# Kernel optimization log

Hardware: AMD Instinct MI355X
Metric: run time of the kernel (lower is better)

The kernel has to match this reference:

```python
import jax, jax.numpy as jnp
import numpy as np

N_NODES = 50000


def gcn_conv(h, W, b, src, dst, n_nodes):
    # PyG GCNConv: h' = D^{-1/2} (A + I) D^{-1/2} (h @ W) + b
    h = h @ W  # [N, out]
    deg = jax.ops.segment_sum(jnp.ones_like(dst, dtype=h.dtype), dst, num_segments=n_nodes)
    dinv = jnp.where(deg > 0, jax.lax.rsqrt(deg), 0.0)  # [N]
    norm = dinv[src] * dinv[dst]  # [E]
    msg = h[src] * norm[:, None]  # [E, out]
    out = jax.ops.segment_sum(msg, dst, num_segments=n_nodes)
    return out + b


def setup_inputs() -> dict:
    key = jax.random.key(0)
    ks = jax.random.split(key, 12)
    N, E, P, D, H = N_NODES, 1600000, 200000, 128, 128
    s = lambda fan_in: 1.0 / np.sqrt(fan_in)
    return {
        "x": jax.random.normal(ks[0], (N, D), dtype=jnp.float32),
        "edge_index": jax.random.randint(ks[1], (2, E), 0, N, dtype=jnp.int32),
        "drug_pairs": jax.random.randint(ks[2], (P, 2), 0, N, dtype=jnp.int32),
        "W1": jax.random.normal(ks[3], (D, H), dtype=jnp.float32) * s(D),
        "b1": jnp.zeros((H,), dtype=jnp.float32),
        "W2": jax.random.normal(ks[4], (H, H), dtype=jnp.float32) * s(H),
        "b2": jnp.zeros((H,), dtype=jnp.float32),
        "Wh1": jax.random.normal(ks[5], (2 * H, H), dtype=jnp.float32) * s(2 * H),
        "bh1": jnp.zeros((H,), dtype=jnp.float32),
        "Wh2": jax.random.normal(ks[6], (H, 1), dtype=jnp.float32) * s(H),
        "bh2": jnp.zeros((1,), dtype=jnp.float32),
    }


def reference(x, edge_index, drug_pairs, W1, b1, W2, b2, Wh1, bh1, Wh2, bh2):
    n = x.shape[0]
    # add self-loops once (GCNConv default add_self_loops=True)
    loop = jnp.arange(n, dtype=edge_index.dtype)
    src = jnp.concatenate([edge_index[0], loop])
    dst = jnp.concatenate([edge_index[1], loop])

    h = jax.nn.relu(gcn_conv(x, W1, b1, src, dst, n))  # dropout = identity (eval)
    h = jax.nn.relu(gcn_conv(h, W2, b2, src, dst, n))

    combined = jnp.concatenate([h[drug_pairs[:, 0]], h[drug_pairs[:, 1]]], axis=1)  # [P, 2H]
    out = jax.nn.relu(combined @ Wh1 + bh1) @ Wh2 + bh2  # [P, 1]
    return out
```

## Files before the change

kernel.cpp:

```cpp
#include <hip/hip_runtime.h>
#include <hip/hip_fp16.h>


#define BSH 9
#define BSZ (1 << BSH)
#define MSB 4096
#define XPAD 132
#define HB 256

typedef __attribute__((ext_vector_type(8))) short bf16x8;
typedef __attribute__((ext_vector_type(8))) _Float16 f16x8;
typedef __attribute__((ext_vector_type(4))) float f32x4;
typedef __attribute__((ext_vector_type(4))) int i32x4;

__device__ __forceinline__ void acc8(uint4 u, float4& lo, float4& hi) {
  float2 f0 = __half22float2(((const __half2*)&u)[0]);
  float2 f1 = __half22float2(((const __half2*)&u)[1]);
  float2 f2 = __half22float2(((const __half2*)&u)[2]);
  float2 f3 = __half22float2(((const __half2*)&u)[3]);
  lo.x += f0.x; lo.y += f0.y; lo.z += f1.x; lo.w += f1.y;
  hi.x += f2.x; hi.y += f2.y; hi.z += f3.x; hi.w += f3.y;
}

__device__ __forceinline__ void split8(const float* v, bf16x8& hi, bf16x8& lo) {
#pragma unroll
  for (int j = 0; j < 8; ++j) {
    unsigned u = __float_as_uint(v[j]);
    hi[j] = (short)(u >> 16);
    float lf = v[j] - __uint_as_float(u & 0xffff0000u);
    lo[j] = (short)(__float_as_uint(lf) >> 16);
  }
}

__global__ __launch_bounds__(256) void k_prep_hist(
    const float* __restrict__ W1, const float* __restrict__ W2,
    const float* __restrict__ Wh1, short* __restrict__ fragH,
    short* __restrict__ fragL,
    const int* __restrict__ dst, int* __restrict__ gcnt, int e, int kb) {
  if (blockIdx.x >= 32) {
    __shared__ int h4[512];
    int bid = blockIdx.x - 32;
    int tid = threadIdx.x, wid = tid >> 6;
    for (int t = tid; t < 512; t += 256) h4[t] = 0;
    __syncthreads();
    const i32x4* dst4 = (const i32x4*)dst;
    int ne4 = e >> 2;
    const int STR = HB * 256;
    int i = bid * 256 + tid;
    for (; i < ne4 - STR; i += 2 * STR) {
      i32x4 a = __builtin_nontemporal_load(&dst4[i]);
      i32x4 b = __builtin_nontemporal_load(&dst4[i + STR]);
      atomicAdd(&h4[wid * 128 + (a.x >> BSH)], 1);
      atomicAdd(&h4[wid * 128 + (a.y >> BSH)], 1);
      atomicAdd(&h4[wid * 128 + (a.z >> BSH)], 1);
      atomicAdd(&h4[wid * 128 + (a.w >> BSH)], 1);
      atomicAdd(&h4[wid * 128 + (b.x >> BSH)], 1);
      atomicAdd(&h4[wid * 128 + (b.y >> BSH)], 1);
      atomicAdd(&h4[wid * 128 + (b.z >> BSH)], 1);
      atomicAdd(&h4[wid * 128 + (b.w >> BSH)], 1);
    }
    for (; i < ne4; i += STR) {
      i32x4 a = __builtin_nontemporal_load(&dst4[i]);
      atomicAdd(&h4[wid * 128 + (a.x >> BSH)], 1);
      atomicAdd(&h4[wid * 128 + (a.y >> BSH)], 1);
      atomicAdd(&h4[wid * 128 + (a.z >> BSH)], 1);
      atomicAdd(&h4[wid * 128 + (a.w >> BSH)], 1);
    }
    if (bid == 0 && tid < (e & 3)) {
      int d = dst[(ne4 << 2) + tid];
      atomicAdd(&h4[wid * 128 + (d >> BSH)], 1);
    }
    __syncthreads();
    if (tid < kb)
      atomicAdd(&gcnt[tid], h4[tid] + h4[128 + tid] + h4[256 + tid] + h4[384 + tid]);
    return;
  }
  int g = blockIdx.x * 256 + threadIdx.x;
  int w = g >> 11;
  int rem = g & 2047;
  int lane = rem & 63;
  int ts = rem >> 6;
  int t = ts >> 2, s = ts & 3;
  int n = (t << 4) + (lane & 15);
  int k0 = s * 32 + (lane >> 4) * 8;
  const float* W = (w == 0) ? W1 : (w == 1) ? W2 : (w == 2) ? Wh1 : (Wh1 + 128 * 128);
  short h[8], l[8];
#pragma unroll
  for (int j = 0; j < 8; ++j) {
    float x = W[(k0 + j) * 128 + n];
    if (w == 0) {
      unsigned u = __float_as_uint(x);
      h[j] = (short)(u >> 16);
      float lf = x - __uint_as_float(u & 0xffff0000u);
      l[j] = (short)(__float_as_uint(lf) >> 16);
    } else {
      __half hh = __float2half(x);
      h[j] = __half_as_short(hh);
      l[j] = __half_as_short(__float2half(x - __half2float(hh)));
    }
  }
  ((int4*)fragH)[g] = *(int4*)h;
  ((int4*)fragL)[g] = *(int4*)l;
}

__device__ __forceinline__ void gemm1_body(
    const float* __restrict__ X, const short* __restrict__ fragH,
    const short* __restrict__ fragL, __half* __restrict__ C16, int n,
    int bid, float* sX) {
  int tid = threadIdx.x;
  int row0 = bid * 64;
  const float2* X2 = (const float2*)(X + (size_t)row0 * 128);
#pragma unroll
  for (int it = 0; it < 16; ++it) {
    int t = it * 256 + tid;
    int r = t >> 6, c2 = t & 63;
    int gr = row0 + r;
    float2 v = (gr < n) ? X2[t] : make_float2(0.f, 0.f);
    *(float2*)&sX[r * XPAD + c2 * 2] = v;
  }
  __syncthreads();
  int wid = tid >> 6, lane = tid & 63;
  int r0 = row0 + wid * 16;
  if (r0 >= n) return;
  int m = lane & 15, quad = lane >> 4;
  const float* xrow = sX + (wid * 16 + m) * XPAD;
  f32x4 acc[8];
#pragma unroll
  for (int t = 0; t < 8; ++t) acc[t] = (f32x4)(0.f);
  const int4* FH = (const int4*)fragH;
  const int4* FL = (const int4*)fragL;
#pragma unroll
  for (int s = 0; s < 4; ++s) {
    int k0 = s * 32 + quad * 8;
    float xv[8];
    *(float2*)&xv[0] = *(const float2*)(xrow + k0);
    *(float2*)&xv[2] = *(const float2*)(xrow + k0 + 2);
    *(float2*)&xv[4] = *(const float2*)(xrow + k0 + 4);
    *(float2*)&xv[6] = *(const float2*)(xrow + k0 + 6);
    bf16x8 ah, al;
    split8(xv, ah, al);
#pragma unroll
    for (int t = 0; t < 8; ++t) {
      int idx = (t * 4 + s) * 64 + lane;
      bf16x8 bh = *(const bf16x8*)&FH[idx];
      bf16x8 bl = *(const bf16x8*)&FL[idx];
      acc[t] = __builtin_amdgcn_mfma_f32_16x16x32_bf16(ah, bh, acc[t], 0, 0, 0);
      acc[t] = __builtin_amdgcn_mfma_f32_16x16x32_bf16(al, bh, acc[t], 0, 0, 0);
      acc[t] = __builtin_amdgcn_mfma_f32_16x16x32_bf16(ah, bl, acc[t], 0, 0, 0);
    }
  }
#pragma unroll
  for (int t = 0; t < 8; ++t) {
#pragma unroll
    for (int r = 0; r < 4; ++r) {
      int row = r0 + quad * 4 + r;
      C16[(size_t)row * 128 + t * 16 + m] = __float2half(acc[t][r]);
    }
  }
}

__device__ __forceinline__ void multisplit_body(
    const int* __restrict__ src, const int* __restrict__ dst,
    const int* __restrict__ gcnt, int* __restrict__ gcur,
    int* __restrict__ tmp, int e, int kb, int bid, int* lds) {
  int* h4 = lds;
  int* off = lds + 512;
  int* sbase = lds + 1024;
  int* ws = lds + 1152;
  int tid = threadIdx.x, wid = tid >> 6, lane = tid & 63;
  for (int t = tid; t < 512; t += 256) h4[t] = 0;
  __syncthreads();
  int i0 = bid * MSB + tid;
  int d[16], rk[16];
#pragma unroll
  for (int u = 0; u < 16; ++u) {
    int i = i0 + u * 256;
    if (i < e) {
      d[u] = __builtin_nontemporal_load(&dst[i]);
      rk[u] = atomicAdd(&h4[wid * 128 + (d[u] >> BSH)], 1);
    }
  }
  __syncthreads();
  int tot = 0;
  if (tid < 128) {
    int c0 = h4[tid], c1 = h4[128 + tid], c2 = h4[256 + tid], c3 = h4[384 + tid];
    off[tid] = 0; off[128 + tid] = c0;
    off[256 + tid] = c0 + c1; off[384 + tid] = c0 + c1 + c2;
    tot = c0 + c1 + c2 + c3;
  }
  int v = (tid < 128 && tid < kb) ? gcnt[tid] : 0;
  int orig = v;
#pragma unroll
  for (int o = 1; o < 64; o <<= 1) {
    int u = __shfl_up(v, o, 64);
    if (lane >= o) v += u;
  }
  if (lane == 63 && wid < 2) ws[wid] = v;
  __syncthreads();
  if (tid < 128) sbase[tid] = ((wid == 1) ? ws[0] : 0) + v - orig;
  __syncthreads();
  if (tid < kb && tot > 0) sbase[tid] += atomicAdd(&gcur[tid], tot);
  __syncthreads();
#pragma unroll
  for (int u = 0; u < 16; ++u) {
    int i = i0 + u * 256;
    if (i < e) {
      int s = __builtin_nontemporal_load(&src[i]);
      int k = d[u] >> BSH;
      tmp[sbase[k] + off[wid * 128 + k] + rk[u]] = ((d[u] & (BSZ - 1)) << 16) | s;
    }
  }
}

__global__ __launch_bounds__(256) void k_ms_gemm1(
    const int* __restrict__ src, const int* __restrict__ dst,
    const int* __restrict__ gcnt, int* __restrict__ gcur,
    int* __restrict__ tmp, int e, int kb, int msblocks,
    const float* __restrict__ X, const short* __restrict__ fragH,
    const short* __restrict__ fragL, __half* __restrict__ C16, int n) {
  __shared__ float sX[64 * XPAD];
  if ((int)blockIdx.x < msblocks) {
    multisplit_body(src, dst, gcnt, gcur, tmp, e, kb, blockIdx.x, (int*)sX);
    return;
  }
  gemm1_body(X, fragH, fragL, C16, n, blockIdx.x - msblocks, sX);
}

__global__ __launch_bounds__(512) void k_bucket_build(
    const int* __restrict__ tmp, const int* __restrict__ gcnt,
    int* __restrict__ rowptr, float* __restrict__ dinv,
    unsigned short* __restrict__ colarr, __half* __restrict__ g16,
    int n, int kb, int e) {
  __shared__ int dl[BSZ], cl[BSZ], sbase[128], ws[8];
  __shared__ float sdi[BSZ];
  int t = threadIdx.x, b = blockIdx.x;
  int lane = t & 63, w = t >> 6;
  int v = (t < 128 && t < kb) ? gcnt[t] : 0;
  int orig0 = v;
#pragma unroll
  for (int o = 1; o < 64; o <<= 1) {
    int u = __shfl_up(v, o, 64);
    if (lane >= o) v += u;
  }
  if (lane == 63 && w < 2) ws[w] = v;
  dl[t] = 0;
  __syncthreads();
  if (t < 128) sbase[t] = ((w == 1) ? ws[0] : 0) + v - orig0;
  __syncthreads();
  int s0 = sbase[b];
  int s1 = s0 + gcnt[b];
  {
    int j = s0 + t;
    for (; j < s1 - 3584; j += 4096) {
      int v0 = tmp[j];
      int v1 = tmp[j + 512];
      int v2 = tmp[j + 1024];
      int v3 = tmp[j + 1536];
      int v4 = tmp[j + 2048];
      int v5 = tmp[j + 2560];
      int v6 = tmp[j + 3072];
      int v7 = tmp[j + 3584];
      atomicAdd(&dl[((unsigned)v0) >> 16], 1);
      atomicAdd(&dl[((unsigned)v1) >> 16], 1);
      atomicAdd(&dl[((unsigned)v2) >> 16], 1);
      atomicAdd(&dl[((unsigned)v3) >> 16], 1);
      atomicAdd(&dl[((unsigned)v4) >> 16], 1);
      atomicAdd(&dl[((unsigned)v5) >> 16], 1);
      atomicAdd(&dl[((unsigned)v6) >> 16], 1);
      atomicAdd(&dl[((unsigned)v7) >> 16], 1);
    }
    for (; j < s1; j += 512)
      atomicAdd(&dl[((unsigned)tmp[j]) >> 16], 1);
  }
  __syncthreads();
  int dv = dl[t], orig = dv;
#pragma unroll
  for (int o = 1; o < 64; o <<= 1) {
    int u = __shfl_up(dv, o, 64);
    if (lane >= o) dv += u;
  }
  if (lane == 63) ws[w] = dv;
  __syncthreads();
  if (t == 0) {
    int a = 0;
#pragma unroll
    for (int k = 0; k < 8; ++k) { int x = ws[k]; ws[k] = a; a += x; }
  }
  __syncthreads();
  int ex = ws[w] + dv - orig;
  cl[t] = ex;
  int node = (b << BSH) + t;
  float di = rsqrtf((float)(orig + 1));
  sdi[t] = di;
  if (node < n) {
    rowptr[node] = s0 + ex;
    dinv[node] = di;
  }
  if (b == kb - 1 && t == 0) rowptr[n] = e;
  __syncthreads();
  {
    int j = s0 + t;
    for (; j < s1 - 3584; j += 4096) {
      int p0 = tmp[j];
      int p1 = tmp[j + 512];
      int p2 = tmp[j + 1024];
      int p3 = tmp[j + 1536];
      int p4 = tmp[j + 2048];
      int p5 = tmp[j + 2560];
      int p6 = tmp[j + 3072];
      int p7 = tmp[j + 3584];
      int r0 = atomicAdd(&cl[((unsigned)p0) >> 16], 1);
      int r1 = atomicAdd(&cl[((unsigned)p1) >> 16], 1);
      int r2 = atomicAdd(&cl[((unsigned)p2) >> 16], 1);
      int r3 = atomicAdd(&cl[((unsigned)p3) >> 16], 1);
      int r4 = atomicAdd(&cl[((unsigned)p4) >> 16], 1);
      int r5 = atomicAdd(&cl[((unsigned)p5) >> 16], 1);
      int r6 = atomicAdd(&cl[((unsigned)p6) >> 16], 1);
      int r7 = atomicAdd(&cl[((unsigned)p7) >> 16], 1);
      colarr[s0 + r0] = (unsigned short)(p0 & 0xFFFF);
      colarr[s0 + r1] = (unsigned short)(p1 & 0xFFFF);
      colarr[s0 + r2] = (unsigned short)(p2 & 0xFFFF);
      colarr[s0 + r3] = (unsigned short)(p3 & 0xFFFF);
      colarr[s0 + r4] = (unsigned short)(p4 & 0xFFFF);
      colarr[s0 + r5] = (unsigned short)(p5 & 0xFFFF);
      colarr[s0 + r6] = (unsigned short)(p6 & 0xFFFF);
      colarr[s0 + r7] = (unsigned short)(p7 & 0xFFFF);
    }
    for (; j < s1; j += 512) {
      int p = tmp[j];
      int r = atomicAdd(&cl[((unsigned)p) >> 16], 1);
      colarr[s0 + r] = (unsigned short)(p & 0xFFFF);
    }
  }
  {
    int base = b << BSH;
    int rows = n - base;
    if (rows > BSZ) rows = BSZ;
    uint4* G = (uint4*)g16;
    for (int idx = t; idx < rows * 16; idx += 512) {
      int rl = idx >> 4;
      float dsc = sdi[rl];
      size_t gi = (size_t)(base + rl) * 16 + (idx & 15);
      uint4 u = G[gi];
      __half2* hp = (__half2*)&u;
#pragma unroll
      for (int k2 = 0; k2 < 4; ++k2) {
        float2 f = __half22float2(hp[k2]);
        hp[k2] = __floats2half2_rn(f.x * dsc, f.y * dsc);
      }
      G[gi] = u;
    }
  }
}

__global__ __launch_bounds__(256) void k_gemm_f16(
    const __half* __restrict__ X16, const short* __restrict__ fragH,
    const short* __restrict__ fragL, const float* __restrict__ rowscale,
    __half* __restrict__ C16, int n) {
  int wid = threadIdx.x >> 6, lane = threadIdx.x & 63;
  int r0 = (blockIdx.x * 4 + wid) * 16;
  if (r0 >= n) return;
  int m = lane & 15, quad = lane >> 4;
  const uint4* Xr = (const uint4*)(X16 + (size_t)(r0 + m) * 128);
  f32x4 acc[8];
#pragma unroll
  for (int t = 0; t < 8; ++t) acc[t] = (f32x4)(0.f);
  const int4* FH = (const int4*)fragH;
  const int4* FL = (const int4*)fragL;
#pragma unroll
  for (int s = 0; s < 4; ++s) {
    uint4 av = Xr[quad + 4 * s];
    f16x8 a = *(const f16x8*)&av;
#pragma unroll
    for (int t = 0; t < 8; ++t) {
      int idx = (t * 4 + s) * 64 + lane;
      int4 bhv = FH[idx], blv = FL[idx];
      f16x8 bh = *(const f16x8*)&bhv;
      f16x8 bl = *(const f16x8*)&blv;
      acc[t] = __builtin_amdgcn_mfma_f32_16x16x32_f16(a, bh, acc[t], 0, 0, 0);
      acc[t] = __builtin_amdgcn_mfma_f32_16x16x32_f16(a, bl, acc[t], 0, 0, 0);
    }
  }
  float sc[4];
#pragma unroll
  for (int r = 0; r < 4; ++r)
    sc[r] = rowscale ? rowscale[r0 + quad * 4 + r] : 1.f;
#pragma unroll
  for (int t = 0; t < 8; ++t) {
#pragma unroll
    for (int r = 0; r < 4; ++r) {
      int row = r0 + quad * 4 + r;
      C16[(size_t)row * 128 + t * 16 + m] = __float2half(acc[t][r] * sc[r]);
    }
  }
}

__global__ __launch_bounds__(256) void k_gemm_dual_f16(
    const __half* __restrict__ X16,
    const short* __restrict__ fHa, const short* __restrict__ fLa,
    const short* __restrict__ fHb, const short* __restrict__ fLb,
    __half* __restrict__ A16, __half* __restrict__ B16, int n) {
  int wid = threadIdx.x >> 6, lane = threadIdx.x & 63;
  int r0 = (blockIdx.x * 4 + wid) * 16;
  if (r0 >= n) return;
  int m = lane & 15, quad = lane >> 4;
  const uint4* Xr = (const uint4*)(X16 + (size_t)(r0 + m) * 128);
  f32x4 accA[8], accB[8];
#pragma unroll
  for (int t = 0; t < 8; ++t) { accA[t] = (f32x4)(0.f); accB[t] = (f32x4)(0.f); }
  const int4* FHa = (const int4*)fHa; const int4* FLa = (const int4*)fLa;
  const int4* FHb = (const int4*)fHb; const int4* FLb = (const int4*)fLb;
#pragma unroll
  for (int s = 0; s < 4; ++s) {
    uint4 av = Xr[quad + 4 * s];
    f16x8 a = *(const f16x8*)&av;
#pragma unroll
    for (int t = 0; t < 8; ++t) {
      int idx = (t * 4 + s) * 64 + lane;
      int4 v0 = FHa[idx], v1 = FLa[idx], v2 = FHb[idx], v3 = FLb[idx];
      accA[t] = __builtin_amdgcn_mfma_f32_16x16x32_f16(a, *(const f16x8*)&v0, accA[t], 0, 0, 0);
      accA[t] = __builtin_amdgcn_mfma_f32_16x16x32_f16(a, *(const f16x8*)&v1, accA[t], 0, 0, 0);
      accB[t] = __builtin_amdgcn_mfma_f32_16x16x32_f16(a, *(const f16x8*)&v2, accB[t], 0, 0, 0);
      accB[t] = __builtin_amdgcn_mfma_f32_16x16x32_f16(a, *(const f16x8*)&v3, accB[t], 0, 0, 0);
    }
  }
#pragma unroll
  for (int t = 0; t < 8; ++t) {
#pragma unroll
    for (int r = 0; r < 4; ++r) {
      int row = r0 + quad * 4 + r;
      A16[(size_t)row * 128 + t * 16 + m] = __float2half(accA[t][r]);
      B16[(size_t)row * 128 + t * 16 + m] = __float2half(accB[t][r]);
    }
  }
}

__global__ __launch_bounds__(256) void k_agg_h(
    const __half2* __restrict__ g2, const float* __restrict__ dinv,
    const int* __restrict__ rowptr, const unsigned short* __restrict__ col,
    const float* __restrict__ bias, __half* __restrict__ out16, int n) {
  int i = blockIdx.x * 4 + (threadIdx.x >> 6);
  if (i >= n) return;
  int lane = threadIdx.x & 63;
  int sub = lane >> 4;
  int c8 = lane & 15;
  const uint4* G = (const uint4*)g2;
  float4 z = make_float4(0.f, 0.f, 0.f, 0.f);
  float4 lo0 = z, lo1 = z, lo2 = z, lo3 = z, hi0 = z, hi1 = z, hi2 = z, hi3 = z;
  if (sub == 0) acc8(G[(size_t)i * 16 + c8], lo0, hi0);
  int beg = rowptr[i], end = rowptr[i + 1];
  int j = beg;
  for (; j + 16 <= end; j += 16) {
    int s0 = __builtin_nontemporal_load(&col[j + sub]);
    int s1 = __builtin_nontemporal_load(&col[j + 4 + sub]);
    int s2 = __builtin_nontemporal_load(&col[j + 8 + sub]);
    int s3 = __builtin_nontemporal_load(&col[j + 12 + sub]);
    uint4 u0 = G[(size_t)s0 * 16 + c8];
    uint4 u1 = G[(size_t)s1 * 16 + c8];
    uint4 u2 = G[(size_t)s2 * 16 + c8];
    uint4 u3 = G[(size_t)s3 * 16 + c8];
    acc8(u0, lo0, hi0); acc8(u1, lo1, hi1);
    acc8(u2, lo2, hi2); acc8(u3, lo3, hi3);
  }
  for (; j + 4 <= end; j += 4) {
    int s0 = __builtin_nontemporal_load(&col[j + sub]);
    acc8(G[(size_t)s0 * 16 + c8], lo1, hi1);
  }
  int rem = end - j;
  if (sub < rem) {
    int s0 = __builtin_nontemporal_load(&col[j + sub]);
    acc8(G[(size_t)s0 * 16 + c8], lo2, hi2);
  }
  float4 lo, hi;
  lo.x = (lo0.x + lo1.x) + (lo2.x + lo3.x);
  lo.y = (lo0.y + lo1.y) + (lo2.y + lo3.y);
  lo.z = (lo0.z + lo1.z) + (lo2.z + lo3.z);
  lo.w = (lo0.w + lo1.w) + (lo2.w + lo3.w);
  hi.x = (hi0.x + hi1.x) + (hi2.x + hi3.x);
  hi.y = (hi0.y + hi1.y) + (hi2.y + hi3.y);
  hi.z = (hi0.z + hi1.z) + (hi2.z + hi3.z);
  hi.w = (hi0.w + hi1.w) + (hi2.w + hi3.w);
  lo.x += __shfl_down(lo.x, 32, 64); lo.x += __shfl_down(lo.x, 16, 64);
  lo.y += __shfl_down(lo.y, 32, 64); lo.y += __shfl_down(lo.y, 16, 64);
  lo.z += __shfl_down(lo.z, 32, 64); lo.z += __shfl_down(lo.z, 16, 64);
  lo.w += __shfl_down(lo.w, 32, 64); lo.w += __shfl_down(lo.w, 16, 64);
  hi.x += __shfl_down(hi.x, 32, 64); hi.x += __shfl_down(hi.x, 16, 64);
  hi.y += __shfl_down(hi.y, 32, 64); hi.y += __shfl_down(hi.y, 16, 64);
  hi.z += __shfl_down(hi.z, 32, 64); hi.z += __shfl_down(hi.z, 16, 64);
  hi.w += __shfl_down(hi.w, 32, 64); hi.w += __shfl_down(hi.w, 16, 64);
  if (sub == 0) {
    float di = dinv[i];
    float4 b0 = ((const float4*)bias)[2 * c8];
    float4 b1 = ((const float4*)bias)[2 * c8 + 1];
    __half2 q0 = __floats2half2_rn(fmaxf(fmaf(di, lo.x, b0.x), 0.f),
                                   fmaxf(fmaf(di, lo.y, b0.y), 0.f));
    __half2 q1 = __floats2half2_rn(fmaxf(fmaf(di, lo.z, b0.z), 0.f),
                                   fmaxf(fmaf(di, lo.w, b0.w), 0.f));
    __half2 q2 = __floats2half2_rn(fmaxf(fmaf(di, hi.x, b1.x), 0.f),
                                   fmaxf(fmaf(di, hi.y, b1.y), 0.f));
    __half2 q3 = __floats2half2_rn(fmaxf(fmaf(di, hi.z, b1.z), 0.f),
                                   fmaxf(fmaf(di, hi.w, b1.w), 0.f));
    uint4 o;
    o.x = *(unsigned*)&q0; o.y = *(unsigned*)&q1;
    o.z = *(unsigned*)&q2; o.w = *(unsigned*)&q3;
    ((uint4*)out16)[(size_t)i * 16 + c8] = o;
  }
}

__global__ __launch_bounds__(256) void k_pairs_h(
    const __half* __restrict__ A, const __half* __restrict__ B,
    const int* __restrict__ pairs, const float* __restrict__ bh1,
    const float* __restrict__ wh2, const float* __restrict__ bh2,
    float* __restrict__ out, int P) {
  int wp = (blockIdx.x * 4 + (threadIdx.x >> 6)) * 4;
  int lane = threadIdx.x & 63;
  int sub = lane >> 4;
  int c8 = lane & 15;
  int pr = sub >> 1;
  int ab = sub & 1;
  const uint4* T = ab ? (const uint4*)B : (const uint4*)A;
  int pA = wp + pr;
  int pB = wp + 2 + pr;
  uint4 u0 = make_uint4(0, 0, 0, 0), u1 = u0;
  if (pA < P) {
    int r = pairs[2 * pA + ab];
    u0 = T[(size_t)r * 16 + c8];
  }
  if (pB < P) {
    int r = pairs[2 * pB + ab];
    u1 = T[(size_t)r * 16 + c8];
  }
  float4 b0 = ((const float4*)bh1)[2 * c8];
  float4 b1 = ((const float4*)bh1)[2 * c8 + 1];
  float4 w0 = ((const float4*)wh2)[2 * c8];
  float4 w1 = ((const float4*)wh2)[2 * c8 + 1];
  float s0, s1;
  {
    float4 lo = make_float4(0, 0, 0, 0), hi = lo;
    acc8(u0, lo, hi);
    lo.x += __shfl_down(lo.x, 16, 64); lo.y += __shfl_down(lo.y, 16, 64);
    lo.z += __shfl_down(lo.z, 16, 64); lo.w += __shfl_down(lo.w, 16, 64);
    hi.x += __shfl_down(hi.x, 16, 64); hi.y += __shfl_down(hi.y, 16, 64);
    hi.z += __shfl_down(hi.z, 16, 64); hi.w += __shfl_down(hi.w, 16, 64);
    s0 = fmaxf(lo.x + b0.x, 0.f) * w0.x + fmaxf(lo.y + b0.y, 0.f) * w0.y +
         fmaxf(lo.z + b0.z, 0.f) * w0.z + fmaxf(lo.w + b0.w, 0.f) * w0.w +
         fmaxf(hi.x + b1.x, 0.f) * w1.x + fmaxf(hi.y + b1.y, 0.f) * w1.y +
         fmaxf(hi.z + b1.z, 0.f) * w1.z + fmaxf(hi.w + b1.w, 0.f) * w1.w;
  }
  {
    float4 lo = make_float4(0, 0, 0, 0), hi = lo;
    acc8(u1, lo, hi);
    lo.x += __shfl_down(lo.x, 16, 64); lo.y += __shfl_down(lo.y, 16, 64);
    lo.z += __shfl_down(lo.z, 16, 64); lo.w += __shfl_down(lo.w, 16, 64);
    hi.x += __shfl_down(hi.x, 16, 64); hi.y += __shfl_down(hi.y, 16, 64);
    hi.z += __shfl_down(hi.z, 16, 64); hi.w += __shfl_down(hi.w, 16, 64);
    s1 = fmaxf(lo.x + b0.x, 0.f) * w0.x + fmaxf(lo.y + b0.y, 0.f) * w0.y +
         fmaxf(lo.z + b0.z, 0.f) * w0.z + fmaxf(lo.w + b0.w, 0.f) * w0.w +
         fmaxf(hi.x + b1.x, 0.f) * w1.x + fmaxf(hi.y + b1.y, 0.f) * w1.y +
         fmaxf(hi.z + b1.z, 0.f) * w1.z + fmaxf(hi.w + b1.w, 0.f) * w1.w;
  }
#pragma unroll
  for (int o = 8; o > 0; o >>= 1) {
    s0 += __shfl_down(s0, o, 64);
    s1 += __shfl_down(s1, o, 64);
  }
  float bb = bh2[0];
  if (lane == 0 && wp < P) out[wp] = s0 + bb;
  if (lane == 32 && wp + 1 < P) out[wp + 1] = s0 + bb;
  if (lane == 0 && wp + 2 < P) out[wp + 2] = s1 + bb;
  if (lane == 32 && wp + 3 < P) out[wp + 3] = s1 + bb;
}

extern "C" void kernel_launch(void* const* d_in, const int* in_sizes, int n_in,
                              void* d_out, int out_size, void* d_ws, size_t ws_size,
                              hipStream_t stream) {
  const float* x   = (const float*)d_in[0];
  const int* ei    = (const int*)d_in[1];
  const int* pairs = (const int*)d_in[2];
  const float* W1  = (const float*)d_in[3];
  const float* b1  = (const float*)d_in[4];
  const float* W2  = (const float*)d_in[5];
  const float* b2  = (const float*)d_in[6];
  const float* Wh1 = (const float*)d_in[7];
  const float* bh1 = (const float*)d_in[8];
  const float* Wh2 = (const float*)d_in[9];
  const float* bh2 = (const float*)d_in[10];
  (void)n_in; (void)out_size; (void)ws_size;

  int N = in_sizes[0] / 128;
  int E = in_sizes[1] / 2;
  int P = in_sizes[2] / 2;
  const int* src = ei;
  const int* dst = ei + E;
  int KB = (N + BSZ - 1) >> BSH;

  char* wsp = (char*)d_ws;
  size_t off = 0;
  auto alloc = [&](size_t bytes) -> void* {
    void* p = wsp + off;
    off += (bytes + 255) & ~(size_t)255;
    return p;
  };
  __half* g16 = (__half*)alloc((size_t)N * 128 * 2);
  __half* h1  = (__half*)alloc((size_t)N * 128 * 2);
  __half* h2  = (__half*)alloc((size_t)N * 128 * 2);
  float* dinv = (float*)alloc((size_t)N * 4);
  int* rowptr = (int*)alloc((size_t)(N + 1) * 4);
  unsigned short* colarr = (unsigned short*)alloc((size_t)E * 2);
  int* tmp    = (int*)alloc((size_t)E * 4);
  short* fragH = (short*)alloc(4 * 2048 * 8 * 2);
  short* fragL = (short*)alloc(4 * 2048 * 8 * 2);
  int* gc     = (int*)alloc(2 * 128 * 4);
  int* gcnt = gc;
  int* gcur = gc + 128;
  __half* A16 = g16;
  __half* B16 = h1;
  short* fH_W1 = fragH + 0 * 16384;  short* fL_W1 = fragL + 0 * 16384;
  short* fH_W2 = fragH + 1 * 16384;  short* fL_W2 = fragL + 1 * 16384;
  short* fH_Wa = fragH + 2 * 16384;  short* fL_Wa = fragL + 2 * 16384;
  short* fH_Wb = fragH + 3 * 16384;  short* fL_Wb = fragL + 3 * 16384;

  int GB = (N + 63) / 64;
  int GF = (N / 16 + 3) / 4;
  int AB = (N + 3) / 4;
  int MS = (E + MSB - 1) / MSB;

  hipMemsetAsync(gc, 0, 2 * 128 * 4, stream);
  k_prep_hist<<<32 + HB, 256, 0, stream>>>(W1, W2, Wh1, fragH, fragL,
                                           dst, gcnt, E, KB);
  k_ms_gemm1<<<MS + GB, 256, 0, stream>>>(src, dst, gcnt, gcur, tmp, E, KB, MS,
                                          x, fH_W1, fL_W1, g16, N);
  k_bucket_build<<<KB, 512, 0, stream>>>(tmp, gcnt, rowptr, dinv, colarr,
                                         g16, N, KB, E);
  k_agg_h<<<AB, 256, 0, stream>>>((const __half2*)g16, dinv, rowptr, colarr, b1, h1, N);
  k_gemm_f16<<<GF, 256, 0, stream>>>(h1, fH_W2, fL_W2, dinv, g16, N);
  k_agg_h<<<AB, 256, 0, stream>>>((const __half2*)g16, dinv, rowptr, colarr, b2, h2, N);
  k_gemm_dual_f16<<<GF, 256, 0, stream>>>(h2, fH_Wa, fL_Wa, fH_Wb, fL_Wb,
                                          A16, B16, N);
  k_pairs_h<<<(P + 15) / 16, 256, 0, stream>>>(A16, B16, pairs, bh1, Wh2, bh2,
                                               (float*)d_out, P);
}
```

Measured before the change: 336.4 us.

## Fuse pair head GEMM into gather kernel using MFMA on gathered pair rows

Replaces the per-node dual GEMM (h2 @ Wa, h2 @ Wb over all 50k nodes) plus the pair gather kernel with a single kernel. It gathers h2 rows for each pair and runs the MLP head GEMM with MFMA directly per pair, with the weight fragments staged in shared memory. This removes one kernel launch and the write and reread of the two N x 128 intermediates. In exchange it does more MFMA work, since there are 200k pairs against 50k nodes, and it uses 128KB of LDS in 1024-thread blocks, which limits occupancy.

```diff
diff --git a/kernel.cpp b/kernel.cpp
--- a/kernel.cpp
+++ b/kernel.cpp
@@ -391,46 +391,6 @@
     for (int r = 0; r < 4; ++r) {
       int row = r0 + quad * 4 + r;
       C16[(size_t)row * 128 + t * 16 + m] = __float2half(acc[t][r] * sc[r]);
-    }
-  }
-}
-
-__global__ __launch_bounds__(256) void k_gemm_dual_f16(
-    const __half* __restrict__ X16,
-    const short* __restrict__ fHa, const short* __restrict__ fLa,
-    const short* __restrict__ fHb, const short* __restrict__ fLb,
-    __half* __restrict__ A16, __half* __restrict__ B16, int n) {
-  int wid = threadIdx.x >> 6, lane = threadIdx.x & 63;
-  int r0 = (blockIdx.x * 4 + wid) * 16;
-  if (r0 >= n) return;
-  int m = lane & 15, quad = lane >> 4;
-  const uint4* Xr = (const uint4*)(X16 + (size_t)(r0 + m) * 128);
-  f32x4 accA[8], accB[8];
-#pragma unroll
-  for (int t = 0; t < 8; ++t) { accA[t] = (f32x4)(0.f); accB[t] = (f32x4)(0.f); }
-  const int4* FHa = (const int4*)fHa; const int4* FLa = (const int4*)fLa;
-  const int4* FHb = (const int4*)fHb; const int4* FLb = (const int4*)fLb;
-#pragma unroll
-  for (int s = 0; s < 4; ++s) {
-    uint4 av = Xr[quad + 4 * s];
-    f16x8 a = *(const f16x8*)&av;
-#pragma unroll
-    for (int t = 0; t < 8; ++t) {
-      int idx = (t * 4 + s) * 64 + lane;
-      int4 v0 = FHa[idx], v1 = FLa[idx], v2 = FHb[idx], v3 = FLb[idx];
-      accA[t] = __builtin_amdgcn_mfma_f32_16x16x32_f16(a, *(const f16x8*)&v0, accA[t], 0, 0, 0);
-      accA[t] = __builtin_amdgcn_mfma_f32_16x16x32_f16(a, *(const f16x8*)&v1, accA[t], 0, 0, 0);
-      accB[t] = __builtin_amdgcn_mfma_f32_16x16x32_f16(a, *(const f16x8*)&v2, accB[t], 0, 0, 0);
-      accB[t] = __builtin_amdgcn_mfma_f32_16x16x32_f16(a, *(const f16x8*)&v3, accB[t], 0, 0, 0);
-    }
-  }
-#pragma unroll
-  for (int t = 0; t < 8; ++t) {
-#pragma unroll
-    for (int r = 0; r < 4; ++r) {
-      int row = r0 + quad * 4 + r;
-      A16[(size_t)row * 128 + t * 16 + m] = __float2half(accA[t][r]);
-      B16[(size_t)row * 128 + t * 16 + m] = __float2half(accB[t][r]);
     }
   }
 }
@@ -507,68 +467,82 @@
   }
 }
 
-__global__ __launch_bounds__(256) void k_pairs_h(
-    const __half* __restrict__ A, const __half* __restrict__ B,
+__global__ __launch_bounds__(1024) void k_pairs_mfma(
+    const __half* __restrict__ h2,
+    const short* __restrict__ fHa, const short* __restrict__ fLa,
+    const short* __restrict__ fHb, const short* __restrict__ fLb,
     const int* __restrict__ pairs, const float* __restrict__ bh1,
     const float* __restrict__ wh2, const float* __restrict__ bh2,
     float* __restrict__ out, int P) {
-  int wp = (blockIdx.x * 4 + (threadIdx.x >> 6)) * 4;
-  int lane = threadIdx.x & 63;
-  int sub = lane >> 4;
-  int c8 = lane & 15;
-  int pr = sub >> 1;
-  int ab = sub & 1;
-  const uint4* T = ab ? (const uint4*)B : (const uint4*)A;
-  int pA = wp + pr;
-  int pB = wp + 2 + pr;
-  uint4 u0 = make_uint4(0, 0, 0, 0), u1 = u0;
-  if (pA < P) {
-    int r = pairs[2 * pA + ab];
-    u0 = T[(size_t)r * 16 + c8];
-  }
-  if (pB < P) {
-    int r = pairs[2 * pB + ab];
-    u1 = T[(size_t)r * 16 + c8];
-  }
-  float4 b0 = ((const float4*)bh1)[2 * c8];
-  float4 b1 = ((const float4*)bh1)[2 * c8 + 1];
-  float4 w0 = ((const float4*)wh2)[2 * c8];
-  float4 w1 = ((const float4*)wh2)[2 * c8 + 1];
-  float s0, s1;
+  __shared__ int4 sF[4][2048];
   {
-    float4 lo = make_float4(0, 0, 0, 0), hi = lo;
-    acc8(u0, lo, hi);
-    lo.x += __shfl_down(lo.x, 16, 64); lo.y += __shfl_down(lo.y, 16, 64);
-    lo.z += __shfl_down(lo.z, 16, 64); lo.w += __shfl_down(lo.w, 16, 64);
-    hi.x += __shfl_down(hi.x, 16, 64); hi.y += __shfl_down(hi.y, 16, 64);
-    hi.z += __shfl_down(hi.z, 16, 64); hi.w += __shfl_down(hi.w, 16, 64);
-    s0 = fmaxf(lo.x + b0.x, 0.f) * w0.x + fmaxf(lo.y + b0.y, 0.f) * w0.y +
-         fmaxf(lo.z + b0.z, 0.f) * w0.z + fmaxf(lo.w + b0.w, 0.f) * w0.w +
-         fmaxf(hi.x + b1.x, 0.f) * w1.x + fmaxf(hi.y + b1.y, 0.f) * w1.y +
-         fmaxf(hi.z + b1.z, 0.f) * w1.z + fmaxf(hi.w + b1.w, 0.f) * w1.w;
-  }
-  {
-    float4 lo = make_float4(0, 0, 0, 0), hi = lo;
-    acc8(u1, lo, hi);
-    lo.x += __shfl_down(lo.x, 16, 64); lo.y += __shfl_down(lo.y, 16, 64);
-    lo.z += __shfl_down(lo.z, 16, 64); lo.w += __shfl_down(lo.w, 16, 64);
-    hi.x += __shfl_down(hi.x, 16, 64); hi.y += __shfl_down(hi.y, 16, 64);
-    hi.z += __shfl_down(hi.z, 16, 64); hi.w += __shfl_down(hi.w, 16, 64);
-    s1 = fmaxf(lo.x + b0.x, 0.f) * w0.x + fmaxf(lo.y + b0.y, 0.f) * w0.y +
-         fmaxf(lo.z + b0.z, 0.f) * w0.z + fmaxf(lo.w + b0.w, 0.f) * w0.w +
-         fmaxf(hi.x + b1.x, 0.f) * w1.x + fmaxf(hi.y + b1.y, 0.f) * w1.y +
-         fmaxf(hi.z + b1.z, 0.f) * w1.z + fmaxf(hi.w + b1.w, 0.f) * w1.w;
+    const int4* g0 = (const int4*)fHa;
+    const int4* g1 = (const int4*)fLa;
+    const int4* g2 = (const int4*)fHb;
+    const int4* g3 = (const int4*)fLb;
+    for (int t = threadIdx.x; t < 2048; t += 1024) {
+      sF[0][t] = g0[t];
+      sF[1][t] = g1[t];
+      sF[2][t] = g2[t];
+      sF[3][t] = g3[t];
+    }
+  }
+  __syncthreads();
+  int w = threadIdx.x >> 6, lane = threadIdx.x & 63;
+  int m = lane & 15, quad = lane >> 4;
+  int p0 = blockIdx.x * 256 + w * 16;
+  int pm = p0 + m;
+  int iA = 0, jB = 0;
+  if (pm < P) {
+    iA = pairs[2 * pm];
+    jB = pairs[2 * pm + 1];
+  }
+  const __half* ri = h2 + (size_t)iA * 128 + quad * 8;
+  const __half* rj = h2 + (size_t)jB * 128 + quad * 8;
+  f16x8 ai[4], aj[4];
+#pragma unroll
+  for (int s = 0; s < 4; ++s) {
+    ai[s] = *(const f16x8*)(ri + s * 32);
+    aj[s] = *(const f16x8*)(rj + s * 32);
+  }
+  f32x4 acc[8];
+#pragma unroll
+  for (int t = 0; t < 8; ++t) acc[t] = (f32x4)(0.f);
+#pragma unroll
+  for (int s = 0; s < 4; ++s) {
+#pragma unroll
+    for (int t = 0; t < 8; ++t) {
+      int idx = (t * 4 + s) * 64 + lane;
+      int4 vha = sF[0][idx], vla = sF[1][idx];
+      int4 vhb = sF[2][idx], vlb = sF[3][idx];
+      acc[t] = __builtin_amdgcn_mfma_f32_16x16x32_f16(ai[s], *(const f16x8*)&vha, acc[t], 0, 0, 0);
+      acc[t] = __builtin_amdgcn_mfma_f32_16x16x32_f16(ai[s], *(const f16x8*)&vla, acc[t], 0, 0, 0);
+      acc[t] = __builtin_amdgcn_mfma_f32_16x16x32_f16(aj[s], *(const f16x8*)&vhb, acc[t], 0, 0, 0);
+      acc[t] = __builtin_amdgcn_mfma_f32_16x16x32_f16(aj[s], *(const f16x8*)&vlb, acc[t], 0, 0, 0);
+    }
+  }
+  float sP[4] = {0.f, 0.f, 0.f, 0.f};
+#pragma unroll
+  for (int t = 0; t < 8; ++t) {
+    float bb = bh1[t * 16 + m];
+    float ww = wh2[t * 16 + m];
+#pragma unroll
+    for (int r = 0; r < 4; ++r)
+      sP[r] += fmaxf(acc[t][r] + bb, 0.f) * ww;
   }
 #pragma unroll
   for (int o = 8; o > 0; o >>= 1) {
-    s0 += __shfl_down(s0, o, 64);
-    s1 += __shfl_down(s1, o, 64);
-  }
-  float bb = bh2[0];
-  if (lane == 0 && wp < P) out[wp] = s0 + bb;
-  if (lane == 32 && wp + 1 < P) out[wp + 1] = s0 + bb;
-  if (lane == 0 && wp + 2 < P) out[wp + 2] = s1 + bb;
-  if (lane == 32 && wp + 3 < P) out[wp + 3] = s1 + bb;
+#pragma unroll
+    for (int r = 0; r < 4; ++r) sP[r] += __shfl_down(sP[r], o, 64);
+  }
+  if (m == 0) {
+    float bb2 = bh2[0];
+#pragma unroll
+    for (int r = 0; r < 4; ++r) {
+      int p = p0 + quad * 4 + r;
+      if (p < P) out[p] = sP[r] + bb2;
+    }
+  }
 }
 
 extern "C" void kernel_launch(void* const* d_in, const int* in_sizes, int n_in,
@@ -613,8 +587,6 @@
   int* gc     = (int*)alloc(2 * 128 * 4);
   int* gcnt = gc;
   int* gcur = gc + 128;
-  __half* A16 = g16;
-  __half* B16 = h1;
   short* fH_W1 = fragH + 0 * 16384;  short* fL_W1 = fragL + 0 * 16384;
   short* fH_W2 = fragH + 1 * 16384;  short* fL_W2 = fragL + 1 * 16384;
   short* fH_Wa = fragH + 2 * 16384;  short* fL_Wa = fragL + 2 * 16384;
@@ -635,8 +607,7 @@
   k_agg_h<<<AB, 256, 0, stream>>>((const __half2*)g16, dinv, rowptr, colarr, b1, h1, N);
   k_gemm_f16<<<GF, 256, 0, stream>>>(h1, fH_W2, fL_W2, dinv, g16, N);
   k_agg_h<<<AB, 256, 0, stream>>>((const __half2*)g16, dinv, rowptr, colarr, b2, h2, N);
-  k_gemm_dual_f16<<<GF, 256, 0, stream>>>(h2, fH_Wa, fL_Wa, fH_Wb, fL_Wb,
-                                          A16, B16, N);
-  k_pairs_h<<<(P + 15) / 16, 256, 0, stream>>>(A16, B16, pairs, bh1, Wh2, bh2,
-                                               (float*)d_out, P);
-}
+  k_pairs_mfma<<<(P + 255) / 256, 1024, 0, stream>>>(
+      h2, fH_Wa, fL_Wa, fH_Wb, fL_Wb, pairs, bh1, Wh2, bh2,
+      (float*)d_out, P);
+}
```

New measurement: 333.2 us. Within noise of the previous version (-1.0%).
